# Kernel tuning notes

Measured on AMD Instinct MI355X. Metric: run time of the kernel, lower is better.

The kernel has to match this reference:

```python
import jax, jax.numpy as jnp
import numpy as np

DT_RANK = 12


def _mixer(x, in_w, conv_w, conv_b, xproj_w, dt_w, dt_b, A_log, D_skip, out_w):
    # x: [B, L, d_model]
    B, L, _ = x.shape
    d_inner, d_state = A_log.shape
    k = conv_w.shape[-1]
    xz = x @ in_w.T                                  # [B, L, 2*d_inner]
    x_part, z = jnp.split(xz, 2, axis=-1)
    # causal depthwise conv1d (torch pads both sides with k-1 then slices [:L] == left-pad only)
    xc = x_part.transpose(0, 2, 1)                   # [B, d_inner, L]
    xc = jax.lax.conv_general_dilated(
        xc, conv_w, window_strides=(1,), padding=[(k - 1, 0)],
        feature_group_count=d_inner, dimension_numbers=("NCH", "OIH", "NCH"))
    xc = xc + conv_b[None, :, None]
    x_part = jax.nn.silu(xc.transpose(0, 2, 1))      # [B, L, d_inner]
    dt_bc = x_part @ xproj_w.T                       # [B, L, dt_rank + 2*d_state]
    dt_part = dt_bc[..., :DT_RANK]
    b_term = jnp.tanh(dt_bc[..., DT_RANK:DT_RANK + d_state])
    c_term = jnp.tanh(dt_bc[..., DT_RANK + d_state:])
    dt = jax.nn.softplus(dt_part @ dt_w.T + dt_b) + 1e-4   # [B, L, d_inner]
    a = -jnp.exp(A_log)                              # [d_inner, d_state]

    def step(state, inp):
        x_t, dt_t, b_t, c_t = inp                    # [B,di], [B,di], [B,N], [B,N]
        da = jnp.exp(dt_t[:, :, None] * a)           # [B, di, N]
        db = (1.0 - da) * b_t[:, None, :]
        state = da * state + db * x_t[:, :, None]
        y_t = (state * c_t[:, None, :]).sum(-1) + D_skip * x_t
        return state, y_t

    init = jnp.zeros((B, d_inner, d_state), x.dtype)
    xs = (x_part.transpose(1, 0, 2), dt.transpose(1, 0, 2),
          b_term.transpose(1, 0, 2), c_term.transpose(1, 0, 2))
    _, ys = jax.lax.scan(step, init, xs)             # ys: [L, B, d_inner]
    y = ys.transpose(1, 0, 2) * jax.nn.silu(z)
    return y @ out_w.T                               # [B, L, d_model]


def setup_inputs() -> dict:
    key = jax.random.key(0)
    B, L, D = 32, 577, 192
    d_inner, d_state, d_conv = 384, 8, 4
    ks = jax.random.split(key, 16)
    s = 0.02
    inp = {"x": jax.random.normal(ks[0], (B, L, D), jnp.float32)}
    for i, p in enumerate(["fw", "bw"]):
        kk = jax.random.split(ks[1 + i], 8)
        inp[f"{p}_in_w"] = jax.random.normal(kk[0], (2 * d_inner, D), jnp.float32) * s
        inp[f"{p}_conv_w"] = jax.random.normal(kk[1], (d_inner, 1, d_conv), jnp.float32) * 0.1
        inp[f"{p}_conv_b"] = jnp.zeros((d_inner,), jnp.float32)
        inp[f"{p}_xproj_w"] = jax.random.normal(kk[2], (DT_RANK + 2 * d_state, d_inner), jnp.float32) * s
        inp[f"{p}_dt_w"] = jax.random.normal(kk[3], (d_inner, DT_RANK), jnp.float32) * s
        inp[f"{p}_dt_b"] = jnp.zeros((d_inner,), jnp.float32)
        inp[f"{p}_A_log"] = jax.random.uniform(kk[4], (d_inner, d_state), jnp.float32)
        inp[f"{p}_D"] = jnp.ones((d_inner,), jnp.float32)
        inp[f"{p}_out_w"] = jax.random.normal(kk[5], (D, d_inner), jnp.float32) * s
    return inp


def reference(x,
              fw_in_w, fw_conv_w, fw_conv_b, fw_xproj_w, fw_dt_w, fw_dt_b, fw_A_log, fw_D, fw_out_w,
              bw_in_w, bw_conv_w, bw_conv_b, bw_xproj_w, bw_dt_w, bw_dt_b, bw_A_log, bw_D, bw_out_w):
    y_fwd = _mixer(x, fw_in_w, fw_conv_w, fw_conv_b, fw_xproj_w, fw_dt_w, fw_dt_b, fw_A_log, fw_D, fw_out_w)
    x_rev = jnp.flip(x, axis=1)
    y_bwd = _mixer(x_rev, bw_in_w, bw_conv_w, bw_conv_b, bw_xproj_w, bw_dt_w, bw_dt_b, bw_A_log, bw_D, bw_out_w)
    y_bwd = jnp.flip(y_bwd, axis=1)
    return 0.5 * (y_fwd + y_bwd)
```

## Files before the change

### kernel.cpp

```cpp
#include <hip/hip_runtime.h>
#include <hip/hip_bf16.h>

#define L2E 1.44269504088896340f
#define LN2 0.69314718055994531f

typedef __bf16 bf16x8 __attribute__((ext_vector_type(8)));
typedef __bf16 bf16x4 __attribute__((ext_vector_type(4)));
typedef float f32x4 __attribute__((ext_vector_type(4)));

__device__ __forceinline__ float fexp2(float x){ return __builtin_amdgcn_exp2f(x); }
__device__ __forceinline__ float flog2(float x){ return __builtin_amdgcn_logf(x); }
__device__ __forceinline__ float frcp(float x){ return __builtin_amdgcn_rcpf(x); }
__device__ __forceinline__ float fsigmoid(float x){ return frcp(1.f + fexp2(-x*L2E)); }
__device__ __forceinline__ float fsoftplus(float x){
  float sp = flog2(1.f + fexp2(x*L2E))*LN2;
  return (x > 15.f) ? x : sp;
}
__device__ __forceinline__ float ftanh_(float x){
  x = fminf(fmaxf(x, -10.f), 10.f);
  float e = fexp2(2.f*L2E*x);
  return (e - 1.f)*frcp(e + 1.f);
}

#define NB 32
#define LS 577
#define DM 192
#define DI 384
#define BL 18464
#define M2T 36928
#define T_CH 37
#define N_CH 16

__global__ __launch_bounds__(256) void k_prep(
    const float* __restrict__ x,
    const float* __restrict__ fw_in, const float* __restrict__ bw_in,
    const float* __restrict__ fw_out, const float* __restrict__ bw_out,
    const float* __restrict__ fw_xp, const float* __restrict__ bw_xp,
    const float* __restrict__ fw_al, const float* __restrict__ bw_al,
    __hip_bfloat16* __restrict__ xbf, __hip_bfloat16* __restrict__ wcat,
    __hip_bfloat16* __restrict__ wout, __hip_bfloat16* __restrict__ xpp,
    float* __restrict__ alog2)
{
  const int S0 = 3545088;
  const int S1 = S0 + 294912;
  const int S2 = S1 + 147456;
  const int S3 = S2 + 24576;
  const int S4 = S3 + 6144;
  int idx = blockIdx.x*256 + threadIdx.x;
  if (idx < S0) {
    xbf[idx] = __float2bfloat16(x[idx]);
  } else if (idx < S1) {
    int i = idx - S0; int r = i/192, k = i - r*192;
    float v = (r < 768) ? fw_in[r*192+k] : bw_in[(r-768)*192+k];
    wcat[i] = __float2bfloat16(v);
  } else if (idx < S2) {
    int i = idx - S1; int o = i/768, k = i - o*768;
    float v = 0.5f * ((k < 384) ? fw_out[o*384+k] : bw_out[o*384+(k-384)]);
    wout[i] = __float2bfloat16(v);
  } else if (idx < S3) {
    int i = idx - S2; int d = i/12288; int rr = i - d*12288;
    int n = rr/384, k = rr - n*384;
    const float* xp = d ? bw_xp : fw_xp;
    float v = (n < 28) ? xp[n*384+k] : 0.f;
    xpp[i] = __float2bfloat16(v);
  } else if (idx < S4) {
    int i = idx - S3;
    const float* al = (i < 3072) ? fw_al : bw_al;
    int j = (i < 3072) ? i : (i - 3072);
    alog2[i] = -fexp2(al[j]*L2E) * L2E;
  }
}

__global__ __launch_bounds__(256) void k_gemm1(const __hip_bfloat16* __restrict__ A,
                                               const __hip_bfloat16* __restrict__ Bw,
                                               __hip_bfloat16* __restrict__ xg,
                                               __hip_bfloat16* __restrict__ zsb)
{
  const int wid = blockIdx.x*4 + (threadIdx.x >> 6);
  const int lane = threadIdx.x & 63;
  const int tm = wid / 12, tn = wid - tm*12;
  const int m0 = tm*32, n0 = tn*128;
  const int r = lane & 15, q = lane >> 4;
  f32x4 acc[2][8];
  #pragma unroll
  for (int a=0;a<2;++a)
    #pragma unroll
    for (int b=0;b<8;++b) acc[a][b] = (f32x4){0.f,0.f,0.f,0.f};
  const __hip_bfloat16* Ab = A + (size_t)(m0 + r)*192 + q*8;
  const __hip_bfloat16* Bb = Bw + (size_t)(n0 + r)*192 + q*8;
  #pragma unroll 2
  for (int kc = 0; kc < 192; kc += 32) {
    bf16x8 af0 = *(const bf16x8*)(Ab + kc);
    bf16x8 af1 = *(const bf16x8*)(Ab + 16*192 + kc);
    #pragma unroll
    for (int ni=0; ni<8; ++ni) {
      bf16x8 bfv = *(const bf16x8*)(Bb + ni*16*192 + kc);
      acc[0][ni] = __builtin_amdgcn_mfma_f32_16x16x32_bf16(af0, bfv, acc[0][ni], 0,0,0);
      acc[1][ni] = __builtin_amdgcn_mfma_f32_16x16x32_bf16(af1, bfv, acc[1][ni], 0,0,0);
    }
  }
  #pragma unroll
  for (int ni=0; ni<8; ++ni) {
    int colg = n0 + ni*16;
    int cat = colg / 384;
    int d = cat >> 1, isz = cat & 1;
    int c = colg - cat*384 + r;
    __hip_bfloat16* dst = (isz ? zsb : xg) + (size_t)(d*BL)*384 + c;
    #pragma unroll
    for (int mi=0; mi<2; ++mi)
      #pragma unroll
      for (int rg=0; rg<4; ++rg) {
        int row = m0 + mi*16 + q*4 + rg;
        float v = acc[mi][ni][rg];
        if (isz) v = v * fsigmoid(v);
        dst[(size_t)row*384] = __float2bfloat16(v);
      }
  }
}

__global__ __launch_bounds__(256) void k_conv(const __hip_bfloat16* __restrict__ xg,
                                              __hip_bfloat16* __restrict__ xcs,
                                              const float* __restrict__ fw_cw, const float* __restrict__ fw_cb,
                                              const float* __restrict__ bw_cw, const float* __restrict__ bw_cb)
{
  int idx = blockIdx.x*256 + threadIdx.x;
  int token = idx / 96; int g = idx - token*96; int c0 = g*4;
  int d = token / BL; int r2 = token - d*BL;
  int b = r2 / LS; int i = r2 - b*LS;
  const float* cwp = (d ? bw_cw : fw_cw);
  const float* cbp = (d ? bw_cb : fw_cb);
  f32x4 w0 = *(const f32x4*)(cwp + (c0+0)*4);
  f32x4 w1 = *(const f32x4*)(cwp + (c0+1)*4);
  f32x4 w2 = *(const f32x4*)(cwp + (c0+2)*4);
  f32x4 w3 = *(const f32x4*)(cwp + (c0+3)*4);
  f32x4 accv = *(const f32x4*)(cbp + c0);
  const __hip_bfloat16* base = xg + ((size_t)(d*BL + b*LS))*384 + c0;
  #pragma unroll
  for (int j=0;j<4;++j) {
    int iw = d ? (i+3-j) : (i-3+j);
    bool valid = d ? (iw < LS) : (iw >= 0);
    if (valid) {
      bf16x4 xv = *(const bf16x4*)(base + (size_t)iw*384);
      f32x4 wj = (f32x4){w0[j], w1[j], w2[j], w3[j]};
      #pragma unroll
      for (int ch=0; ch<4; ++ch) accv[ch] += wj[ch]*(float)xv[ch];
    }
  }
  bf16x4 outv;
  #pragma unroll
  for (int ch=0; ch<4; ++ch) {
    float s = accv[ch]*fsigmoid(accv[ch]);
    outv[ch] = (__bf16)s;
  }
  *(bf16x4*)(xcs + (size_t)token*384 + c0) = outv;
}

__global__ __launch_bounds__(256) void k_dtbc(const __hip_bfloat16* __restrict__ A,
                                              const __hip_bfloat16* __restrict__ xpp,
                                              float* __restrict__ dtbc)
{
  const int wid = blockIdx.x*4 + (threadIdx.x >> 6);
  if (wid >= 1154) return;
  const int lane = threadIdx.x & 63;
  const int m0 = wid*32;
  const int r = lane & 15, q = lane >> 4;
  const int d = (m0 >= BL) ? 1 : 0;
  const __hip_bfloat16* Bp = xpp + (size_t)d*32*384;
  f32x4 acc[2][2];
  #pragma unroll
  for (int a=0;a<2;++a)
    #pragma unroll
    for (int b=0;b<2;++b) acc[a][b] = (f32x4){0.f,0.f,0.f,0.f};
  const __hip_bfloat16* Ab = A + (size_t)(m0 + r)*384 + q*8;
  const __hip_bfloat16* Bb = Bp + (size_t)r*384 + q*8;
  #pragma unroll
  for (int kc = 0; kc < 384; kc += 32) {
    bf16x8 af0 = *(const bf16x8*)(Ab + kc);
    bf16x8 af1 = *(const bf16x8*)(Ab + 16*384 + kc);
    bf16x8 bf0 = *(const bf16x8*)(Bb + kc);
    bf16x8 bf1 = *(const bf16x8*)(Bb + 16*384 + kc);
    acc[0][0] = __builtin_amdgcn_mfma_f32_16x16x32_bf16(af0, bf0, acc[0][0], 0,0,0);
    acc[0][1] = __builtin_amdgcn_mfma_f32_16x16x32_bf16(af0, bf1, acc[0][1], 0,0,0);
    acc[1][0] = __builtin_amdgcn_mfma_f32_16x16x32_bf16(af1, bf0, acc[1][0], 0,0,0);
    acc[1][1] = __builtin_amdgcn_mfma_f32_16x16x32_bf16(af1, bf1, acc[1][1], 0,0,0);
  }
  #pragma unroll
  for (int mi=0; mi<2; ++mi)
    #pragma unroll
    for (int ni=0; ni<2; ++ni)
      #pragma unroll
      for (int rg=0; rg<4; ++rg) {
        int n = ni*16 + r;
        if (n < 28) {
          int m = m0 + mi*16 + q*4 + rg;
          float v = acc[mi][ni][rg];
          if (n >= 12) v = ftanh_(v);
          int r2 = m - d*BL; int b = r2 / LS; int i = r2 - b*LS;
          int ts = d ? (LS-1-i) : i;
          dtbc[((size_t)((d*NB + b)*LS + ts))*28 + n] = v;
        }
      }
}

__global__ __launch_bounds__(64) void k_scan1(const __hip_bfloat16* __restrict__ xcs,
                                              const float* __restrict__ dtbc,
                                              const float* __restrict__ fw_dtw, const float* __restrict__ fw_dtb,
                                              const float* __restrict__ bw_dtw, const float* __restrict__ bw_dtb,
                                              const float* __restrict__ alog2,
                                              float* __restrict__ ps)
{
  const int bid = blockIdx.x;
  const int lane = threadIdx.x;
  const int kc = bid & 15; const int dbc = bid >> 4;
  const int cchunk = dbc % 6; const int db = dbc / 6;
  const int b = db & 31; const int d = db >> 5;
  const int c = cchunk*64 + lane;

  const float* dtwp = (d ? bw_dtw : fw_dtw) + c*12;
  float dtw[12];
  #pragma unroll
  for (int r2=0;r2<12;++r2) dtw[r2] = dtwp[r2];
  const float dtb = (d ? bw_dtb : fw_dtb)[c];
  float al[8];
  const float* alp = alog2 + ((size_t)(d*384 + c))*8;
  #pragma unroll
  for (int s=0;s<8;++s) al[s] = alp[s];

  const float* dtbase = dtbc + ((size_t)((d*NB+b)*LS))*28;
  const __hip_bfloat16* xcb = xcs + ((size_t)(d*BL + b*LS))*384 + c;

  const int ts0 = kc*T_CH;
  const int ts1 = (ts0 + T_CH < LS) ? (ts0 + T_CH) : LS;

  float P[8], S[8];
  #pragma unroll
  for (int s=0;s<8;++s){ P[s]=1.f; S[s]=0.f; }

  float nb[20]; float xnb;
  {
    const float* p0 = dtbase + (size_t)ts0*28;
    #pragma unroll
    for (int k=0;k<20;++k) nb[k] = p0[k];
    int i = d ? (LS-1-ts0) : ts0;
    xnb = __bfloat162float(xcb[(size_t)i*384]);
  }
  for (int ts=ts0; ts<ts1; ++ts) {
    float cur[20];
    #pragma unroll
    for (int k=0;k<20;++k) cur[k] = nb[k];
    float xt = xnb;
    if (ts+1 < ts1) {
      const float* p1 = dtbase + (size_t)(ts+1)*28;
      #pragma unroll
      for (int k=0;k<20;++k) nb[k] = p1[k];
      int i2 = d ? (LS-2-ts) : (ts+1);
      xnb = __bfloat162float(xcb[(size_t)i2*384]);
    }
    float dtr = dtb;
    #pragma unroll
    for (int r2=0;r2<12;++r2) dtr += cur[r2]*dtw[r2];
    float dt = fsoftplus(dtr) + 1e-4f;
    #pragma unroll
    for (int s=0;s<8;++s) {
      float da = fexp2(dt * al[s]);
      float tmp = cur[12+s]*xt;
      S[s] = tmp + da*(S[s]-tmp);
      P[s] *= da;
    }
  }
  float* pp = ps + ((size_t)bid*16)*64 + lane;
  #pragma unroll
  for (int s=0;s<8;++s) pp[s*64] = P[s];
  #pragma unroll
  for (int s=0;s<8;++s) pp[(8+s)*64] = S[s];
}

__global__ __launch_bounds__(64) void k_comb(const float* __restrict__ ps,
                                             float* __restrict__ initst)
{
  const int dbc = blockIdx.x;
  const int lane = threadIdx.x;
  float st[8];
  #pragma unroll
  for (int s=0;s<8;++s) st[s]=0.f;
  for (int kc=0;kc<N_CH;++kc) {
    const float* pp = ps + ((size_t)(dbc*16+kc)*16)*64 + lane;
    float* ip = initst + ((size_t)(dbc*16+kc)*8)*64 + lane;
    #pragma unroll
    for (int s=0;s<8;++s) ip[s*64] = st[s];
    #pragma unroll
    for (int s=0;s<8;++s) {
      float P = pp[s*64], Sv = pp[(8+s)*64];
      st[s] = P*st[s] + Sv;
    }
  }
}

__global__ __launch_bounds__(64) void k_scan2(const __hip_bfloat16* __restrict__ xcs,
                                              const __hip_bfloat16* __restrict__ zsb,
                                              const float* __restrict__ dtbc,
                                              const float* __restrict__ initst,
                                              const float* __restrict__ fw_dtw, const float* __restrict__ fw_dtb,
                                              const float* __restrict__ fw_D,
                                              const float* __restrict__ bw_dtw, const float* __restrict__ bw_dtb,
                                              const float* __restrict__ bw_D,
                                              const float* __restrict__ alog2,
                                              __hip_bfloat16* __restrict__ ybf)
{
  const int bid = blockIdx.x;
  const int lane = threadIdx.x;
  const int kc = bid & 15; const int dbc = bid >> 4;
  const int cchunk = dbc % 6; const int db = dbc / 6;
  const int b = db & 31; const int d = db >> 5;
  const int c = cchunk*64 + lane;

  const float* dtwp = (d ? bw_dtw : fw_dtw) + c*12;
  float dtw[12];
  #pragma unroll
  for (int r2=0;r2<12;++r2) dtw[r2] = dtwp[r2];
  const float dtb = (d ? bw_dtb : fw_dtb)[c];
  const float Dc  = (d ? bw_D : fw_D)[c];
  float al[8];
  const float* alp = alog2 + ((size_t)(d*384 + c))*8;
  #pragma unroll
  for (int s=0;s<8;++s) al[s] = alp[s];

  float st[8];
  {
    const float* ip = initst + ((size_t)bid*8)*64 + lane;
    #pragma unroll
    for (int s=0;s<8;++s) st[s] = ip[s*64];
  }

  const float* dtbase = dtbc + ((size_t)((d*NB+b)*LS))*28;
  const __hip_bfloat16* xcb = xcs + ((size_t)(d*BL + b*LS))*384 + c;
  const __hip_bfloat16* zcb = zsb + ((size_t)(d*BL + b*LS))*384 + c;
  __hip_bfloat16* ybase = ybf + (size_t)(b*LS)*768 + d*384 + c;

  const int ts0 = kc*T_CH;
  const int ts1 = (ts0 + T_CH < LS) ? (ts0 + T_CH) : LS;

  float nb[28]; float xnb, znb;
  {
    const float* p0 = dtbase + (size_t)ts0*28;
    #pragma unroll
    for (int k=0;k<28;++k) nb[k] = p0[k];
    int i = d ? (LS-1-ts0) : ts0;
    xnb = __bfloat162float(xcb[(size_t)i*384]);
    znb = __bfloat162float(zcb[(size_t)i*384]);
  }
  for (int ts=ts0; ts<ts1; ++ts) {
    float cur[28];
    #pragma unroll
    for (int k=0;k<28;++k) cur[k] = nb[k];
    float xt = xnb, zs = znb;
    int i = d ? (LS-1-ts) : ts;
    if (ts+1 < ts1) {
      const float* p1 = dtbase + (size_t)(ts+1)*28;
      #pragma unroll
      for (int k=0;k<28;++k) nb[k] = p1[k];
      int i2 = d ? (LS-2-ts) : (ts+1);
      xnb = __bfloat162float(xcb[(size_t)i2*384]);
      znb = __bfloat162float(zcb[(size_t)i2*384]);
    }
    float dtr = dtb;
    #pragma unroll
    for (int r2=0;r2<12;++r2) dtr += cur[r2]*dtw[r2];
    float dt = fsoftplus(dtr) + 1e-4f;
    float y = Dc * xt;
    #pragma unroll
    for (int s=0;s<8;++s) {
      float da = fexp2(dt * al[s]);
      float tmp = cur[12+s]*xt;
      st[s] = tmp + da*(st[s]-tmp);
      y += st[s]*cur[20+s];
    }
    ybase[(size_t)i*768] = __float2bfloat16(y*zs);
  }
}

__global__ __launch_bounds__(256) void k_gemm2(const __hip_bfloat16* __restrict__ A,
                                               const __hip_bfloat16* __restrict__ Bw,
                                               float* __restrict__ C)
{
  const int wid = blockIdx.x*4 + (threadIdx.x >> 6);
  if (wid >= 1731) return;
  const int lane = threadIdx.x & 63;
  const int tm = wid / 3, tn = wid - tm*3;
  const int m0 = tm*32, n0 = tn*64;
  const int r = lane & 15, q = lane >> 4;
  f32x4 acc[2][4];
  #pragma unroll
  for (int a=0;a<2;++a)
    #pragma unroll
    for (int b=0;b<4;++b) acc[a][b] = (f32x4){0.f,0.f,0.f,0.f};
  const __hip_bfloat16* Ab = A + (size_t)(m0 + r)*768 + q*8;
  const __hip_bfloat16* Bb = Bw + (size_t)(n0 + r)*768 + q*8;
  #pragma unroll 4
  for (int kc = 0; kc < 768; kc += 32) {
    bf16x8 af0 = *(const bf16x8*)(Ab + kc);
    bf16x8 af1 = *(const bf16x8*)(Ab + 16*768 + kc);
    bf16x8 bf0 = *(const bf16x8*)(Bb + kc);
    bf16x8 bf1 = *(const bf16x8*)(Bb + 16*768 + kc);
    bf16x8 bf2 = *(const bf16x8*)(Bb + 32*768 + kc);
    bf16x8 bf3 = *(const bf16x8*)(Bb + 48*768 + kc);
    acc[0][0] = __builtin_amdgcn_mfma_f32_16x16x32_bf16(af0, bf0, acc[0][0], 0,0,0);
    acc[0][1] = __builtin_amdgcn_mfma_f32_16x16x32_bf16(af0, bf1, acc[0][1], 0,0,0);
    acc[0][2] = __builtin_amdgcn_mfma_f32_16x16x32_bf16(af0, bf2, acc[0][2], 0,0,0);
    acc[0][3] = __builtin_amdgcn_mfma_f32_16x16x32_bf16(af0, bf3, acc[0][3], 0,0,0);
    acc[1][0] = __builtin_amdgcn_mfma_f32_16x16x32_bf16(af1, bf0, acc[1][0], 0,0,0);
    acc[1][1] = __builtin_amdgcn_mfma_f32_16x16x32_bf16(af1, bf1, acc[1][1], 0,0,0);
    acc[1][2] = __builtin_amdgcn_mfma_f32_16x16x32_bf16(af1, bf2, acc[1][2], 0,0,0);
    acc[1][3] = __builtin_amdgcn_mfma_f32_16x16x32_bf16(af1, bf3, acc[1][3], 0,0,0);
  }
  #pragma unroll
  for (int mi=0; mi<2; ++mi)
    #pragma unroll
    for (int ni=0; ni<4; ++ni)
      #pragma unroll
      for (int rg=0; rg<4; ++rg) {
        int row = m0 + mi*16 + q*4 + rg;
        int col = n0 + ni*16 + r;
        C[(size_t)row*192 + col] = acc[mi][ni][rg];
      }
}

extern "C" void kernel_launch(void* const* d_in, const int* in_sizes, int n_in,
                              void* d_out, int out_size, void* d_ws, size_t ws_size,
                              hipStream_t stream) {
  const float* x        = (const float*)d_in[0];
  const float* fw_in_w  = (const float*)d_in[1];
  const float* fw_cw    = (const float*)d_in[2];
  const float* fw_cb    = (const float*)d_in[3];
  const float* fw_xp    = (const float*)d_in[4];
  const float* fw_dtw   = (const float*)d_in[5];
  const float* fw_dtb   = (const float*)d_in[6];
  const float* fw_al    = (const float*)d_in[7];
  const float* fw_D     = (const float*)d_in[8];
  const float* fw_ow    = (const float*)d_in[9];
  const float* bw_in_w  = (const float*)d_in[10];
  const float* bw_cw    = (const float*)d_in[11];
  const float* bw_cb    = (const float*)d_in[12];
  const float* bw_xp    = (const float*)d_in[13];
  const float* bw_dtw   = (const float*)d_in[14];
  const float* bw_dtb   = (const float*)d_in[15];
  const float* bw_al    = (const float*)d_in[16];
  const float* bw_D     = (const float*)d_in[17];
  const float* bw_ow    = (const float*)d_in[18];

  char* ws = (char*)d_ws;
  __hip_bfloat16* xbf  = (__hip_bfloat16*)(ws + 0);
  __hip_bfloat16* wcat = (__hip_bfloat16*)(ws + 7090176);
  __hip_bfloat16* wout = (__hip_bfloat16*)(ws + 7680000);
  __hip_bfloat16* xpp  = (__hip_bfloat16*)(ws + 7974912);
  float* alog2         = (float*)(ws + 8024064);
  float* ps            = (float*)(ws + 8048640);
  float* initst        = (float*)(ws + 33214464);
  __hip_bfloat16* ybf  = (__hip_bfloat16*)(ws + 45797376);
  __hip_bfloat16* xg   = (__hip_bfloat16*)(ws + 74158080);
  __hip_bfloat16* xcs  = (__hip_bfloat16*)(ws + 121491456);
  __hip_bfloat16* zsb  = (__hip_bfloat16*)(ws + 149852160);
  float* dtbc          = (float*)(ws + 178212864);

  hipLaunchKernelGGL(k_prep, dim3(15696), dim3(256), 0, stream,
                     x, fw_in_w, bw_in_w, fw_ow, bw_ow, fw_xp, bw_xp, fw_al, bw_al,
                     xbf, wcat, wout, xpp, alog2);
  hipLaunchKernelGGL(k_gemm1, dim3(1731), dim3(256), 0, stream, xbf, wcat, xg, zsb);
  hipLaunchKernelGGL(k_conv, dim3(13848), dim3(256), 0, stream,
                     xg, xcs, fw_cw, fw_cb, bw_cw, bw_cb);
  hipLaunchKernelGGL(k_dtbc, dim3(289), dim3(256), 0, stream, xcs, xpp, dtbc);
  hipLaunchKernelGGL(k_scan1, dim3(6144), dim3(64), 0, stream,
                     xcs, dtbc, fw_dtw, fw_dtb, bw_dtw, bw_dtb, alog2, ps);
  hipLaunchKernelGGL(k_comb, dim3(384), dim3(64), 0, stream, ps, initst);
  hipLaunchKernelGGL(k_scan2, dim3(6144), dim3(64), 0, stream,
                     xcs, zsb, dtbc, initst,
                     fw_dtw, fw_dtb, fw_D, bw_dtw, bw_dtb, bw_D, alog2, ybf);
  hipLaunchKernelGGL(k_gemm2, dim3(433), dim3(256), 0, stream, ybf, wout, (float*)d_out);
}
```

Measured before the change: 334.8 us.

## Tile gemm1 through LDS with 128x128 blocks and coalesced staged output

Rewrites the input-projection GEMM so each block of four waves stages 128x96 slices of A and B into shared memory and computes a 128x128 tile. Each wave holds a 64x64 accumulator. This replaces per-wave direct global loads of 32x128 tiles, which re-read B heavily, and cuts global traffic. The epilogue also goes through LDS, so results are written as coalesced 16-byte rows instead of strided scalar bf16 stores. In exchange it adds more synchronisation and LDS use per block, which may lower occupancy, and it clamps rows past the end for the partial last tile.

```diff
diff --git a/kernel.cpp b/kernel.cpp
--- a/kernel.cpp
+++ b/kernel.cpp
@@ -71,50 +71,89 @@
   }
 }
 
+#define G1_LDA 104
+#define G1_LDO 136
 __global__ __launch_bounds__(256) void k_gemm1(const __hip_bfloat16* __restrict__ A,
                                                const __hip_bfloat16* __restrict__ Bw,
                                                __hip_bfloat16* __restrict__ xg,
                                                __hip_bfloat16* __restrict__ zsb)
 {
-  const int wid = blockIdx.x*4 + (threadIdx.x >> 6);
-  const int lane = threadIdx.x & 63;
-  const int tm = wid / 12, tn = wid - tm*12;
-  const int m0 = tm*32, n0 = tn*128;
+  __shared__ __align__(16) __bf16 smem[26624];
+  __bf16* ldsA = smem;
+  __bf16* ldsB = smem + 128*G1_LDA;
+
+  const int t = threadIdx.x;
+  const int tm = blockIdx.x / 12, tn = blockIdx.x - tm*12;
+  const int m0 = tm*128, n0 = tn*128;
+  const int w = t >> 6, lane = t & 63;
+  const int wr = (w >> 1)*64, wc = (w & 1)*64;
   const int r = lane & 15, q = lane >> 4;
-  f32x4 acc[2][8];
-  #pragma unroll
-  for (int a=0;a<2;++a)
-    #pragma unroll
-    for (int b=0;b<8;++b) acc[a][b] = (f32x4){0.f,0.f,0.f,0.f};
-  const __hip_bfloat16* Ab = A + (size_t)(m0 + r)*192 + q*8;
-  const __hip_bfloat16* Bb = Bw + (size_t)(n0 + r)*192 + q*8;
-  #pragma unroll 2
-  for (int kc = 0; kc < 192; kc += 32) {
-    bf16x8 af0 = *(const bf16x8*)(Ab + kc);
-    bf16x8 af1 = *(const bf16x8*)(Ab + 16*192 + kc);
-    #pragma unroll
-    for (int ni=0; ni<8; ++ni) {
-      bf16x8 bfv = *(const bf16x8*)(Bb + ni*16*192 + kc);
-      acc[0][ni] = __builtin_amdgcn_mfma_f32_16x16x32_bf16(af0, bfv, acc[0][ni], 0,0,0);
-      acc[1][ni] = __builtin_amdgcn_mfma_f32_16x16x32_bf16(af1, bfv, acc[1][ni], 0,0,0);
-    }
-  }
-  #pragma unroll
-  for (int ni=0; ni<8; ++ni) {
-    int colg = n0 + ni*16;
-    int cat = colg / 384;
-    int d = cat >> 1, isz = cat & 1;
-    int c = colg - cat*384 + r;
-    __hip_bfloat16* dst = (isz ? zsb : xg) + (size_t)(d*BL)*384 + c;
-    #pragma unroll
-    for (int mi=0; mi<2; ++mi)
+
+  f32x4 acc[4][4];
+  #pragma unroll
+  for (int a=0;a<4;++a)
+    #pragma unroll
+    for (int b=0;b<4;++b) acc[a][b] = (f32x4){0.f,0.f,0.f,0.f};
+
+  #pragma unroll
+  for (int h=0; h<2; ++h) {
+    if (h) __syncthreads();
+    #pragma unroll
+    for (int j=0;j<6;++j) {
+      int cid = t + 256*j;
+      int row = cid/12; int c8 = (cid - row*12)*8;
+      int gr = m0 + row; if (gr > BL-1) gr = BL-1;
+      bf16x8 va = *(const bf16x8*)(A + (size_t)gr*192 + h*96 + c8);
+      *(bf16x8*)(ldsA + row*G1_LDA + c8) = va;
+      bf16x8 vb = *(const bf16x8*)(Bw + (size_t)(n0+row)*192 + h*96 + c8);
+      *(bf16x8*)(ldsB + row*G1_LDA + c8) = vb;
+    }
+    __syncthreads();
+    #pragma unroll
+    for (int kc=0; kc<96; kc+=32) {
+      bf16x8 af[4], bfv[4];
+      #pragma unroll
+      for (int mi=0; mi<4; ++mi)
+        af[mi] = *(const bf16x8*)(ldsA + (wr + mi*16 + r)*G1_LDA + q*8 + kc);
+      #pragma unroll
+      for (int ni=0; ni<4; ++ni)
+        bfv[ni] = *(const bf16x8*)(ldsB + (wc + ni*16 + r)*G1_LDA + q*8 + kc);
+      #pragma unroll
+      for (int mi=0; mi<4; ++mi)
+        #pragma unroll
+        for (int ni=0; ni<4; ++ni)
+          acc[mi][ni] = __builtin_amdgcn_mfma_f32_16x16x32_bf16(af[mi], bfv[ni], acc[mi][ni], 0,0,0);
+    }
+  }
+
+  const int cat = tn/3;
+  const int cbase = (tn - cat*3)*128;
+  const int d = cat >> 1, isz = cat & 1;
+  __syncthreads();
+  __bf16* ldsO = smem;
+  #pragma unroll
+  for (int mi=0; mi<4; ++mi)
+    #pragma unroll
+    for (int ni=0; ni<4; ++ni)
       #pragma unroll
       for (int rg=0; rg<4; ++rg) {
-        int row = m0 + mi*16 + q*4 + rg;
+        int row = wr + mi*16 + q*4 + rg;
+        int col = wc + ni*16 + r;
         float v = acc[mi][ni][rg];
         if (isz) v = v * fsigmoid(v);
-        dst[(size_t)row*384] = __float2bfloat16(v);
+        ldsO[row*G1_LDO + col] = (__bf16)v;
       }
+  __syncthreads();
+  __hip_bfloat16* dst = (isz ? zsb : xg) + (size_t)(d*BL)*384 + cbase;
+  const int c8 = (t & 15)*8;
+  #pragma unroll
+  for (int it=0; it<8; ++it) {
+    int row = (t >> 4) + it*16;
+    int grow = m0 + row;
+    if (grow < BL) {
+      bf16x8 v = *(const bf16x8*)(ldsO + row*G1_LDO + c8);
+      *(bf16x8*)(dst + (size_t)grow*384 + c8) = v;
+    }
   }
 }
 
@@ -465,7 +504,7 @@
   hipLaunchKernelGGL(k_prep, dim3(15696), dim3(256), 0, stream,
                      x, fw_in_w, bw_in_w, fw_ow, bw_ow, fw_xp, bw_xp, fw_al, bw_al,
                      xbf, wcat, wout, xpp, alog2);
-  hipLaunchKernelGGL(k_gemm1, dim3(1731), dim3(256), 0, stream, xbf, wcat, xg, zsb);
+  hipLaunchKernelGGL(k_gemm1, dim3(1740), dim3(256), 0, stream, xbf, wcat, xg, zsb);
   hipLaunchKernelGGL(k_conv, dim3(13848), dim3(256), 0, stream,
                      xg, xcs, fw_cw, fw_cb, bw_cw, bw_cb);
   hipLaunchKernelGGL(k_dtbc, dim3(289), dim3(256), 0, stream, xcs, xpp, dtbc);
```

Measured after the change: 304.7 us. 9.0% less time.
